# Kernel tuning notes

Measured on AMD Instinct MI355X. Metric: run time of the kernel, lower is better.

Reference implementation:

```python
import jax, jax.numpy as jnp
import numpy as np

HEAD_NUM = 8
KEY_DIM = 16
EMBEDDING_DIM = 128
LOGIT_CLIPPING = 10.0

B, G, P, E = 512, 100, 100, 128


def setup_inputs() -> dict:
    key = jax.random.key(0)
    ks = jax.random.split(key, 9)
    return {
        "input1": jax.random.normal(ks[0], (B, 1, E), jnp.float32),
        "input2": jax.random.normal(ks[1], (B, G, E), jnp.float32),
        "remaining_loaded": jax.random.uniform(ks[2], (B, G, 1), jnp.float32),
        "ninf_mask": jnp.zeros((B, G, P), jnp.float32),
        "encoded_nodes": jax.random.normal(ks[3], (B, P, E), jnp.float32),
        "Wq": jax.random.normal(ks[4], (2 * E + 1, HEAD_NUM * KEY_DIM), jnp.float32) * 0.05,
        "Wk": jax.random.normal(ks[5], (E, HEAD_NUM * KEY_DIM), jnp.float32) * 0.05,
        "Wv": jax.random.normal(ks[6], (E, HEAD_NUM * KEY_DIM), jnp.float32) * 0.05,
        "Wc": jax.random.normal(ks[7], (HEAD_NUM * KEY_DIM, E), jnp.float32) * 0.05,
        "bc": jnp.zeros((E,), jnp.float32),
    }


def _heads(x):  # [B, N, H*K] -> [B, H, N, K]
    b, n, _ = x.shape
    return x.reshape(b, n, HEAD_NUM, KEY_DIM).transpose(0, 2, 1, 3)


def reference(input1, input2, remaining_loaded, ninf_mask, encoded_nodes, Wq, Wk, Wv, Wc, bc):
    group_s = input2.shape[1]
    # reset(): precompute keys/values from encoded nodes
    k = _heads(encoded_nodes @ Wk)  # [B,H,P,K]
    v = _heads(encoded_nodes @ Wv)  # [B,H,P,K]
    # forward()
    input_cat = jnp.concatenate(
        [jnp.broadcast_to(input1, (input1.shape[0], group_s, input1.shape[2])),
         input2, remaining_loaded], axis=2)  # [B,G,2E+1]
    q = _heads(input_cat @ Wq)  # [B,H,G,K]
    # multi-head attention with additive ninf mask
    score = jnp.einsum("bhgk,bhpk->bhgp", q, k) / np.sqrt(KEY_DIM).astype(np.float32)
    score = score + ninf_mask[:, None, :, :]
    weights = jax.nn.softmax(score, axis=3)
    out = jnp.einsum("bhgp,bhpk->bhgk", weights, v)  # [B,H,G,K]
    out_concat = out.transpose(0, 2, 1, 3).reshape(out.shape[0], group_s, HEAD_NUM * KEY_DIM)
    mh_atten_out = out_concat @ Wc + bc  # [B,G,E]
    # single-head pointer scoring with tanh clipping
    score2 = jnp.einsum("bge,bpe->bgp", mh_atten_out, encoded_nodes) / np.sqrt(EMBEDDING_DIM).astype(np.float32)
    score_masked = LOGIT_CLIPPING * jnp.tanh(score2) + ninf_mask
    probs = jax.nn.softmax(score_masked, axis=2)
    return probs
```

## Files before the change

### kernel.cpp

```cpp
#include <hip/hip_runtime.h>

#define NB 512
#define NG 100
#define NP 100
#define NE 128
#define NH 8
#define LDST 136

typedef __attribute__((ext_vector_type(8))) short short8;
typedef __attribute__((ext_vector_type(4))) short short4v;
typedef __attribute__((ext_vector_type(4))) float f32x4;

__device__ __forceinline__ short f2bf(float f) {
    union { float f; unsigned u; } v; v.f = f;
    unsigned r = v.u + 0x7FFFu + ((v.u >> 16) & 1u);
    return (short)(r >> 16);
}

__global__ void prep_kernel(const float* __restrict__ Wq, const float* __restrict__ Wk,
                            const float* __restrict__ Wv, const float* __restrict__ Wc,
                            short* __restrict__ WqT2, short* __restrict__ WkT,
                            short* __restrict__ WvT, short* __restrict__ WcT,
                            float* __restrict__ wqlast)
{
    int idx = blockIdx.x * 256 + threadIdx.x;
    int mat = idx >> 14;
    int e   = idx & 16383;
    int k = e >> 7, n = e & 127;
    float v;
    short* dst;
    if (mat == 0)      { v = Wq[(128 + k) * 128 + n]; dst = WqT2; }
    else if (mat == 1) { v = Wk[k * 128 + n];         dst = WkT;  }
    else if (mat == 2) { v = Wv[k * 128 + n];         dst = WvT;  }
    else               { v = Wc[k * 128 + n];         dst = WcT;  }
    dst[n * 128 + k] = f2bf(v);
    if (idx < 128) wqlast[idx] = Wq[256 * 128 + idx];
}

__global__ __launch_bounds__(512, 2)
void fused_kernel(const float* __restrict__ input1, const float* __restrict__ input2,
                  const float* __restrict__ rem, const float* __restrict__ mask,
                  const float* __restrict__ enc, const float* __restrict__ Wq,
                  const float* __restrict__ bc,
                  const short* __restrict__ WqT2, const short* __restrict__ WkT,
                  const short* __restrict__ WvT, const short* __restrict__ WcT,
                  const float* __restrict__ wqlast, float* __restrict__ out)
{
    extern __shared__ short smem[];
    short* sEnc = smem;
    short* sK   = sEnc + 100 * LDST;
    short* sQ   = sK   + 100 * LDST;
    short* sVT  = sQ   + 100 * LDST;
    short* sWs  = sVT  + 128 * LDST;
    float* sQ1  = (float*)(sWs + 8 * 16 * LDST);

    const int b    = blockIdx.x;
    const int tid  = threadIdx.x;
    const int wave = tid >> 6, lane = tid & 63;
    const int l16  = lane & 15, lh = lane >> 4;

    {
        const float4* e4 = (const float4*)(enc    + (size_t)b * NP * NE);
        const float4* i4 = (const float4*)(input2 + (size_t)b * NG * NE);
        for (int idx = tid; idx < 100 * 32; idx += 512) {
            int row = idx >> 5, c = idx & 31;
            float4 v = e4[idx];
            short4v h = { f2bf(v.x), f2bf(v.y), f2bf(v.z), f2bf(v.w) };
            *(short4v*)(sEnc + row * LDST + c * 4) = h;
            float4 w = i4[idx];
            short4v h2 = { f2bf(w.x), f2bf(w.y), f2bf(w.z), f2bf(w.w) };
            *(short4v*)(sVT + row * LDST + c * 4) = h2;
        }
        {
            int n = tid & 127, part = tid >> 7;
            const float* i1 = input1 + (size_t)b * NE;
            float s = 0.f;
            #pragma unroll 8
            for (int k = part * 32; k < part * 32 + 32; ++k)
                s += i1[k] * Wq[k * NE + n];
            sQ1[part * 128 + n] = s;
        }
    }
    __syncthreads();

    for (int t = wave; t < 56; t += 8) {
        int mt = t >> 3, nt = t & 7;
        f32x4 acc = {0.f, 0.f, 0.f, 0.f};
        #pragma unroll
        for (int ks = 0; ks < 4; ++ks) {
            short8 a = *(const short8*)(sVT + (mt * 16 + l16) * LDST + ks * 32 + lh * 8);
            short8 w = *(const short8*)(WqT2 + (nt * 16 + l16) * NE + ks * 32 + lh * 8);
            acc = __builtin_amdgcn_mfma_f32_16x16x32_bf16(a, w, acc, 0, 0, 0);
        }
        int n = nt * 16 + l16;
        float q1n = sQ1[n] + sQ1[128 + n] + sQ1[256 + n] + sQ1[384 + n];
        float wl = wqlast[n];
        #pragma unroll
        for (int r = 0; r < 4; ++r) {
            int g = mt * 16 + lh * 4 + r;
            if (g < NG) {
                float rv = rem[(size_t)b * NG + g];
                sQ[g * LDST + n] = f2bf(acc[r] + q1n + rv * wl);
            }
        }
    }
    __syncthreads();

    for (int t = wave; t < 112; t += 8) {
        int isV = t >= 56;
        int tt = t - (isV ? 56 : 0);
        int mt = tt >> 3, nt = tt & 7;
        const short* WT = isV ? WvT : WkT;
        f32x4 acc = {0.f, 0.f, 0.f, 0.f};
        #pragma unroll
        for (int ks = 0; ks < 4; ++ks) {
            short8 a = *(const short8*)(sEnc + (mt * 16 + l16) * LDST + ks * 32 + lh * 8);
            short8 w = *(const short8*)(WT + (nt * 16 + l16) * NE + ks * 32 + lh * 8);
            acc = __builtin_amdgcn_mfma_f32_16x16x32_bf16(a, w, acc, 0, 0, 0);
        }
        int n = nt * 16 + l16;
        if (!isV) {
            #pragma unroll
            for (int r = 0; r < 4; ++r) {
                int p = mt * 16 + lh * 4 + r;
                if (p < NP) sK[p * LDST + n] = f2bf(acc[r]);
            }
        } else {
            int p0 = mt * 16 + lh * 4;
            if (p0 < NP) {
                short4v h = { f2bf(acc[0]), f2bf(acc[1]), f2bf(acc[2]), f2bf(acc[3]) };
                *(short4v*)(sVT + n * LDST + p0) = h;
            }
        }
    }
    for (int idx = tid; idx < 128 * 36; idx += 512) {
        int n = idx / 36, c = 100 + idx % 36;
        sVT[n * LDST + c] = 0;
    }
    __syncthreads();

    float mk[7][4];
    if (wave < 7) {
        const int gt = wave;
        #pragma unroll
        for (int pt = 0; pt < 7; ++pt)
            #pragma unroll
            for (int r = 0; r < 4; ++r) {
                int g = gt * 16 + lh * 4 + r, p = pt * 16 + l16;
                mk[pt][r] = (g < NG && p < NP) ? mask[((size_t)b * NG + g) * NP + p]
                                               : -__builtin_inff();
            }
        short* myW = sWs + wave * 16 * LDST;
        for (int i = lane; i < 16 * 24; i += 64) {
            int rr = i / 24, c = 112 + i % 24;
            myW[rr * LDST + c] = 0;
        }

        for (int h = 0; h < NH; ++h) {
            short8 aq = {0,0,0,0,0,0,0,0};
            if (lh < 2) aq = *(const short8*)(sQ + (gt * 16 + l16) * LDST + h * 16 + lh * 8);
            f32x4 sc[7];
            #pragma unroll
            for (int pt = 0; pt < 7; ++pt) {
                short8 kk = {0,0,0,0,0,0,0,0};
                if (lh < 2) kk = *(const short8*)(sK + (pt * 16 + l16) * LDST + h * 16 + lh * 8);
                f32x4 z = {0.f, 0.f, 0.f, 0.f};
                sc[pt] = __builtin_amdgcn_mfma_f32_16x16x32_bf16(aq, kk, z, 0, 0, 0);
            }
            float vals[7][4];
            #pragma unroll
            for (int pt = 0; pt < 7; ++pt) {
                bool pv = (pt * 16 + l16) < NP;
                #pragma unroll
                for (int r = 0; r < 4; ++r)
                    vals[pt][r] = pv ? sc[pt][r] * 0.25f + mk[pt][r] : -__builtin_inff();
            }
            #pragma unroll
            for (int r = 0; r < 4; ++r) {
                float m = vals[0][r];
                #pragma unroll
                for (int pt = 1; pt < 7; ++pt) m = fmaxf(m, vals[pt][r]);
                #pragma unroll
                for (int d = 1; d < 16; d <<= 1) m = fmaxf(m, __shfl_xor(m, d, 64));
                float s = 0.f;
                #pragma unroll
                for (int pt = 0; pt < 7; ++pt) {
                    float e = ((pt * 16 + l16) < NP) ? __expf(vals[pt][r] - m) : 0.f;
                    vals[pt][r] = e; s += e;
                }
                #pragma unroll
                for (int d = 1; d < 16; d <<= 1) s += __shfl_xor(s, d, 64);
                float inv = 1.f / s;
                #pragma unroll
                for (int pt = 0; pt < 7; ++pt) vals[pt][r] *= inv;
            }
            #pragma unroll
            for (int pt = 0; pt < 7; ++pt)
                #pragma unroll
                for (int r = 0; r < 4; ++r)
                    myW[(lh * 4 + r) * LDST + pt * 16 + l16] = f2bf(vals[pt][r]);
            f32x4 o = {0.f, 0.f, 0.f, 0.f};
            #pragma unroll
            for (int ps = 0; ps < 4; ++ps) {
                short8 a  = *(const short8*)(myW + l16 * LDST + ps * 32 + lh * 8);
                short8 vv = *(const short8*)(sVT + (h * 16 + l16) * LDST + ps * 32 + lh * 8);
                o = __builtin_amdgcn_mfma_f32_16x16x32_bf16(a, vv, o, 0, 0, 0);
            }
            #pragma unroll
            for (int r = 0; r < 4; ++r) {
                int g = gt * 16 + lh * 4 + r;
                if (g < NG) sQ[g * LDST + h * 16 + l16] = f2bf(o[r]);
            }
        }
    }
    __syncthreads();

    for (int t = wave; t < 56; t += 8) {
        int mt = t >> 3, nt = t & 7;
        f32x4 acc = {0.f, 0.f, 0.f, 0.f};
        #pragma unroll
        for (int ks = 0; ks < 4; ++ks) {
            short8 a = *(const short8*)(sQ + (mt * 16 + l16) * LDST + ks * 32 + lh * 8);
            short8 w = *(const short8*)(WcT + (nt * 16 + l16) * NE + ks * 32 + lh * 8);
            acc = __builtin_amdgcn_mfma_f32_16x16x32_bf16(a, w, acc, 0, 0, 0);
        }
        int n = nt * 16 + l16;
        float bias = bc[n];
        #pragma unroll
        for (int r = 0; r < 4; ++r) {
            int g = mt * 16 + lh * 4 + r;
            if (g < NG) sK[g * LDST + n] = f2bf(acc[r] + bias);
        }
    }
    __syncthreads();

    if (wave < 7) {
        const int gt = wave;
        short8 afr[4];
        #pragma unroll
        for (int ks = 0; ks < 4; ++ks)
            afr[ks] = *(const short8*)(sK + (gt * 16 + l16) * LDST + ks * 32 + lh * 8);
        float vals[7][4];
        #pragma unroll
        for (int pt = 0; pt < 7; ++pt) {
            f32x4 acc = {0.f, 0.f, 0.f, 0.f};
            #pragma unroll
            for (int ks = 0; ks < 4; ++ks) {
                short8 e8 = *(const short8*)(sEnc + (pt * 16 + l16) * LDST + ks * 32 + lh * 8);
                acc = __builtin_amdgcn_mfma_f32_16x16x32_bf16(afr[ks], e8, acc, 0, 0, 0);
            }
            bool pv = (pt * 16 + l16) < NP;
            #pragma unroll
            for (int r = 0; r < 4; ++r) {
                float x = acc[r] * 0.08838834764831845f;
                float th = 1.f - 2.f / (__expf(2.f * x) + 1.f);
                vals[pt][r] = pv ? 10.f * th + mk[pt][r] : -__builtin_inff();
            }
        }
        #pragma unroll
        for (int r = 0; r < 4; ++r) {
            float m = vals[0][r];
            #pragma unroll
            for (int pt = 1; pt < 7; ++pt) m = fmaxf(m, vals[pt][r]);
            #pragma unroll
            for (int d = 1; d < 16; d <<= 1) m = fmaxf(m, __shfl_xor(m, d, 64));
            float s = 0.f;
            #pragma unroll
            for (int pt = 0; pt < 7; ++pt) {
                float e = ((pt * 16 + l16) < NP) ? __expf(vals[pt][r] - m) : 0.f;
                vals[pt][r] = e; s += e;
            }
            #pragma unroll
            for (int d = 1; d < 16; d <<= 1) s += __shfl_xor(s, d, 64);
            float inv = 1.f / s;
            #pragma unroll
            for (int pt = 0; pt < 7; ++pt) vals[pt][r] *= inv;
        }
        #pragma unroll
        for (int pt = 0; pt < 7; ++pt) {
            int p = pt * 16 + l16;
            if (p < NP) {
                #pragma unroll
                for (int r = 0; r < 4; ++r) {
                    int g = gt * 16 + lh * 4 + r;
                    if (g < NG) out[((size_t)b * NG + g) * NP + p] = vals[pt][r];
                }
            }
        }
    }
}

#define SMEM_BYTES ((3 * 100 * LDST + 128 * LDST + 8 * 16 * LDST) * 2 + 512 * 4)

extern "C" void kernel_launch(void* const* d_in, const int* in_sizes, int n_in,
                              void* d_out, int out_size, void* d_ws, size_t ws_size,
                              hipStream_t stream)
{
    const float* input1 = (const float*)d_in[0];
    const float* input2 = (const float*)d_in[1];
    const float* rem    = (const float*)d_in[2];
    const float* mask   = (const float*)d_in[3];
    const float* enc    = (const float*)d_in[4];
    const float* Wq     = (const float*)d_in[5];
    const float* Wk     = (const float*)d_in[6];
    const float* Wv     = (const float*)d_in[7];
    const float* Wc     = (const float*)d_in[8];
    const float* bc     = (const float*)d_in[9];

    short* WqT2   = (short*)d_ws;
    short* WkT    = WqT2 + 16384;
    short* WvT    = WkT + 16384;
    short* WcT    = WvT + 16384;
    float* wqlast = (float*)(WcT + 16384);

    prep_kernel<<<256, 256, 0, stream>>>(Wq, Wk, Wv, Wc, WqT2, WkT, WvT, WcT, wqlast);

    hipFuncSetAttribute((const void*)fused_kernel,
                        hipFuncAttributeMaxDynamicSharedMemorySize, SMEM_BYTES);
    fused_kernel<<<NB, 512, SMEM_BYTES, stream>>>(
        input1, input2, rem, mask, enc, Wq, bc,
        WqT2, WkT, WvT, WcT, wqlast, (float*)d_out);
}
```

Before: 210.4 us.

## Keep per-wave Q/attention/output in registers with transposed MFMA and swizzled LDS

Result: slower. 321.5 us (+52.8%).

```diff
diff --git a/kernel.cpp b/kernel.cpp
--- a/kernel.cpp
+++ b/kernel.cpp
@@ -5,11 +5,19 @@
 #define NP 100
 #define NE 128
 #define NH 8
-#define LDST 136
 
 typedef __attribute__((ext_vector_type(8))) short short8;
 typedef __attribute__((ext_vector_type(4))) short short4v;
 typedef __attribute__((ext_vector_type(4))) float f32x4;
+
+#define SE_STRIDE 128
+#define SK_STRIDE 128
+#define SVT_STRIDE 112
+#define SE_BASE 0
+#define SK_BASE (100 * 128)
+#define SVT_BASE (SK_BASE + 100 * 128)
+#define SMEM_SHORTS (SVT_BASE + 128 * 112)
+#define SMEM_BYTES (SMEM_SHORTS * 2 + 256 * 4)
 
 __device__ __forceinline__ short f2bf(float f) {
     union { float f; unsigned u; } v; v.f = f;
@@ -17,11 +25,27 @@
     return (short)(r >> 16);
 }
 
+__device__ __forceinline__ f32x4 mfma16(short4v a, short4v b, f32x4 c) {
+#if __has_builtin(__builtin_amdgcn_mfma_f32_16x16x16_bf16)
+    return __builtin_amdgcn_mfma_f32_16x16x16_bf16(a, b, c, 0, 0, 0);
+#elif __has_builtin(__builtin_amdgcn_mfma_f32_16x16x16bf16_1k)
+    return __builtin_amdgcn_mfma_f32_16x16x16bf16_1k(a, b, c, 0, 0, 0);
+#else
+    f32x4 d;
+    asm volatile("v_mfma_f32_16x16x16_bf16 %0, %1, %2, %3"
+                 : "=&v"(d) : "v"(a), "v"(b), "v"(c));
+    return d;
+#endif
+}
+
+__device__ __forceinline__ f32x4 mfma32(short8 a, short8 b, f32x4 c) {
+    return __builtin_amdgcn_mfma_f32_16x16x32_bf16(a, b, c, 0, 0, 0);
+}
+
 __global__ void prep_kernel(const float* __restrict__ Wq, const float* __restrict__ Wk,
                             const float* __restrict__ Wv, const float* __restrict__ Wc,
                             short* __restrict__ WqT2, short* __restrict__ WkT,
-                            short* __restrict__ WvT, short* __restrict__ WcT,
-                            float* __restrict__ wqlast)
+                            short* __restrict__ WvT, short* __restrict__ WcT)
 {
     int idx = blockIdx.x * 256 + threadIdx.x;
     int mat = idx >> 14;
@@ -34,263 +58,253 @@
     else if (mat == 2) { v = Wv[k * 128 + n];         dst = WvT;  }
     else               { v = Wc[k * 128 + n];         dst = WcT;  }
     dst[n * 128 + k] = f2bf(v);
-    if (idx < 128) wqlast[idx] = Wq[256 * 128 + idx];
-}
-
-__global__ __launch_bounds__(512, 2)
+}
+
+__global__ __launch_bounds__(448, 4)
 void fused_kernel(const float* __restrict__ input1, const float* __restrict__ input2,
                   const float* __restrict__ rem, const float* __restrict__ mask,
                   const float* __restrict__ enc, const float* __restrict__ Wq,
                   const float* __restrict__ bc,
                   const short* __restrict__ WqT2, const short* __restrict__ WkT,
                   const short* __restrict__ WvT, const short* __restrict__ WcT,
-                  const float* __restrict__ wqlast, float* __restrict__ out)
+                  float* __restrict__ out)
 {
     extern __shared__ short smem[];
-    short* sEnc = smem;
-    short* sK   = sEnc + 100 * LDST;
-    short* sQ   = sK   + 100 * LDST;
-    short* sVT  = sQ   + 100 * LDST;
-    short* sWs  = sVT  + 128 * LDST;
-    float* sQ1  = (float*)(sWs + 8 * 16 * LDST);
+    float* sQ1 = (float*)(smem + SMEM_SHORTS);
 
     const int b    = blockIdx.x;
     const int tid  = threadIdx.x;
     const int wave = tid >> 6, lane = tid & 63;
     const int l16  = lane & 15, lh = lane >> 4;
+    const int gt   = wave;
+    const int g    = gt * 16 + l16;
+    const bool gok = (g < NG);
+    const float NINF = -__builtin_inff();
 
     {
-        const float4* e4 = (const float4*)(enc    + (size_t)b * NP * NE);
-        const float4* i4 = (const float4*)(input2 + (size_t)b * NG * NE);
-        for (int idx = tid; idx < 100 * 32; idx += 512) {
+        const f32x4* e4 = (const f32x4*)(enc + (size_t)b * NP * NE);
+        for (int idx = tid; idx < NP * 32; idx += 448) {
             int row = idx >> 5, c = idx & 31;
-            float4 v = e4[idx];
-            short4v h = { f2bf(v.x), f2bf(v.y), f2bf(v.z), f2bf(v.w) };
-            *(short4v*)(sEnc + row * LDST + c * 4) = h;
-            float4 w = i4[idx];
-            short4v h2 = { f2bf(w.x), f2bf(w.y), f2bf(w.z), f2bf(w.w) };
-            *(short4v*)(sVT + row * LDST + c * 4) = h2;
-        }
-        {
-            int n = tid & 127, part = tid >> 7;
-            const float* i1 = input1 + (size_t)b * NE;
+            f32x4 v = e4[idx];
+            short4v h = { f2bf(v[0]), f2bf(v[1]), f2bf(v[2]), f2bf(v[3]) };
+            int off = (row * SE_STRIDE + c * 4) ^ ((row & 15) << 2);
+            *(short4v*)(smem + SE_BASE + off) = h;
+        }
+        for (int idx = tid; idx < 128 * 3; idx += 448) {
+            int row = idx / 3, c = 100 + (idx % 3) * 4;
+            int off = (row * SVT_STRIDE + c) ^ ((row & 15) << 2);
+            *(short4v*)(smem + SVT_BASE + off) = (short4v){0, 0, 0, 0};
+        }
+        if (tid < 256) {
+            int part = tid >> 7, n = tid & 127;
+            const float* i1 = input1 + (size_t)b * NE + part * 64;
+            const float* wq = Wq + (size_t)part * 64 * NE + n;
             float s = 0.f;
             #pragma unroll 8
-            for (int k = part * 32; k < part * 32 + 32; ++k)
-                s += i1[k] * Wq[k * NE + n];
+            for (int k = 0; k < 64; ++k) s += i1[k] * wq[k * NE];
             sQ1[part * 128 + n] = s;
         }
     }
     __syncthreads();
 
-    for (int t = wave; t < 56; t += 8) {
-        int mt = t >> 3, nt = t & 7;
+    for (int t = wave; t < 112; t += 7) {
+        int mat = (t >= 56);
+        int tt  = mat ? t - 56 : t;
+        int mt = tt >> 3, nt = tt & 7;
+        const short* WT = mat ? WvT : WkT;
+        int arow = mt * 16 + l16;
+        bool aok = (arow < NP);
         f32x4 acc = {0.f, 0.f, 0.f, 0.f};
         #pragma unroll
-        for (int ks = 0; ks < 4; ++ks) {
-            short8 a = *(const short8*)(sVT + (mt * 16 + l16) * LDST + ks * 32 + lh * 8);
-            short8 w = *(const short8*)(WqT2 + (nt * 16 + l16) * NE + ks * 32 + lh * 8);
-            acc = __builtin_amdgcn_mfma_f32_16x16x32_bf16(a, w, acc, 0, 0, 0);
-        }
-        int n = nt * 16 + l16;
-        float q1n = sQ1[n] + sQ1[128 + n] + sQ1[256 + n] + sQ1[384 + n];
-        float wl = wqlast[n];
-        #pragma unroll
-        for (int r = 0; r < 4; ++r) {
-            int g = mt * 16 + lh * 4 + r;
-            if (g < NG) {
-                float rv = rem[(size_t)b * NG + g];
-                sQ[g * LDST + n] = f2bf(acc[r] + q1n + rv * wl);
-            }
-        }
-    }
-    __syncthreads();
-
-    for (int t = wave; t < 112; t += 8) {
-        int isV = t >= 56;
-        int tt = t - (isV ? 56 : 0);
-        int mt = tt >> 3, nt = tt & 7;
-        const short* WT = isV ? WvT : WkT;
-        f32x4 acc = {0.f, 0.f, 0.f, 0.f};
-        #pragma unroll
-        for (int ks = 0; ks < 4; ++ks) {
-            short8 a = *(const short8*)(sEnc + (mt * 16 + l16) * LDST + ks * 32 + lh * 8);
-            short8 w = *(const short8*)(WT + (nt * 16 + l16) * NE + ks * 32 + lh * 8);
-            acc = __builtin_amdgcn_mfma_f32_16x16x32_bf16(a, w, acc, 0, 0, 0);
-        }
-        int n = nt * 16 + l16;
-        if (!isV) {
+        for (int kt = 0; kt < 8; ++kt) {
+            short4v a = {0, 0, 0, 0};
+            if (aok) {
+                int off = (arow * SE_STRIDE + kt * 16 + lh * 4) ^ ((arow & 15) << 2);
+                a = *(const short4v*)(smem + SE_BASE + off);
+            }
+            short4v w = *(const short4v*)(WT + (nt * 16 + l16) * NE + kt * 16 + lh * 4);
+            acc = mfma16(a, w, acc);
+        }
+        if (!mat) {
             #pragma unroll
             for (int r = 0; r < 4; ++r) {
                 int p = mt * 16 + lh * 4 + r;
-                if (p < NP) sK[p * LDST + n] = f2bf(acc[r]);
+                if (p < NP) {
+                    int off = (p * SK_STRIDE + nt * 16 + l16) ^ ((p & 15) << 2);
+                    smem[SK_BASE + off] = f2bf(acc[r]);
+                }
             }
         } else {
+            int vrow = nt * 16 + l16;
             int p0 = mt * 16 + lh * 4;
             if (p0 < NP) {
                 short4v h = { f2bf(acc[0]), f2bf(acc[1]), f2bf(acc[2]), f2bf(acc[3]) };
-                *(short4v*)(sVT + n * LDST + p0) = h;
-            }
-        }
-    }
-    for (int idx = tid; idx < 128 * 36; idx += 512) {
-        int n = idx / 36, c = 100 + idx % 36;
-        sVT[n * LDST + c] = 0;
+                int off = (vrow * SVT_STRIDE + p0) ^ ((vrow & 15) << 2);
+                *(short4v*)(smem + SVT_BASE + off) = h;
+            }
+        }
+    }
+
+    short4v qb[8];
+    {
+        const float* xrow = input2 + ((size_t)b * NG + g) * NE;
+        short8 xb[4];
+        #pragma unroll
+        for (int ks = 0; ks < 4; ++ks) {
+            f32x4 v0 = {0.f,0.f,0.f,0.f}, v1 = {0.f,0.f,0.f,0.f};
+            if (gok) {
+                v0 = *(const f32x4*)(xrow + ks * 32 + lh * 8);
+                v1 = *(const f32x4*)(xrow + ks * 32 + lh * 8 + 4);
+            }
+            xb[ks] = (short8){ f2bf(v0[0]), f2bf(v0[1]), f2bf(v0[2]), f2bf(v0[3]),
+                               f2bf(v1[0]), f2bf(v1[1]), f2bf(v1[2]), f2bf(v1[3]) };
+        }
+        float remv = gok ? rem[(size_t)b * NG + g] : 0.f;
+        #pragma unroll
+        for (int nt = 0; nt < 8; ++nt) {
+            f32x4 acc = {0.f, 0.f, 0.f, 0.f};
+            #pragma unroll
+            for (int ks = 0; ks < 4; ++ks) {
+                short8 a = *(const short8*)(WqT2 + (nt * 16 + l16) * NE + ks * 32 + lh * 8);
+                acc = mfma32(a, xb[ks], acc);
+            }
+            f32x4 q1a = *(const f32x4*)(sQ1 + nt * 16 + lh * 4);
+            f32x4 q1b = *(const f32x4*)(sQ1 + 128 + nt * 16 + lh * 4);
+            f32x4 wlv = *(const f32x4*)(Wq + 256 * NE + nt * 16 + lh * 4);
+            short4v q;
+            #pragma unroll
+            for (int r = 0; r < 4; ++r)
+                q[r] = f2bf(0.25f * (acc[r] + q1a[r] + q1b[r] + remv * wlv[r]));
+            qb[nt] = q;
+        }
+    }
+
+    float mk[7][4];
+    {
+        const float* mrow = mask + ((size_t)b * NG + g) * NP;
+        #pragma unroll
+        for (int pt = 0; pt < 7; ++pt)
+            #pragma unroll
+            for (int r = 0; r < 4; ++r) {
+                int p = pt * 16 + lh * 4 + r;
+                mk[pt][r] = (gok && p < NP) ? mrow[p] : NINF;
+            }
     }
     __syncthreads();
 
-    float mk[7][4];
-    if (wave < 7) {
-        const int gt = wave;
-        #pragma unroll
-        for (int pt = 0; pt < 7; ++pt)
-            #pragma unroll
-            for (int r = 0; r < 4; ++r) {
-                int g = gt * 16 + lh * 4 + r, p = pt * 16 + l16;
-                mk[pt][r] = (g < NG && p < NP) ? mask[((size_t)b * NG + g) * NP + p]
-                                               : -__builtin_inff();
-            }
-        short* myW = sWs + wave * 16 * LDST;
-        for (int i = lane; i < 16 * 24; i += 64) {
-            int rr = i / 24, c = 112 + i % 24;
-            myW[rr * LDST + c] = 0;
-        }
-
-        for (int h = 0; h < NH; ++h) {
-            short8 aq = {0,0,0,0,0,0,0,0};
-            if (lh < 2) aq = *(const short8*)(sQ + (gt * 16 + l16) * LDST + h * 16 + lh * 8);
-            f32x4 sc[7];
-            #pragma unroll
-            for (int pt = 0; pt < 7; ++pt) {
-                short8 kk = {0,0,0,0,0,0,0,0};
-                if (lh < 2) kk = *(const short8*)(sK + (pt * 16 + l16) * LDST + h * 16 + lh * 8);
-                f32x4 z = {0.f, 0.f, 0.f, 0.f};
-                sc[pt] = __builtin_amdgcn_mfma_f32_16x16x32_bf16(aq, kk, z, 0, 0, 0);
-            }
-            float vals[7][4];
-            #pragma unroll
-            for (int pt = 0; pt < 7; ++pt) {
-                bool pv = (pt * 16 + l16) < NP;
-                #pragma unroll
-                for (int r = 0; r < 4; ++r)
-                    vals[pt][r] = pv ? sc[pt][r] * 0.25f + mk[pt][r] : -__builtin_inff();
-            }
-            #pragma unroll
-            for (int r = 0; r < 4; ++r) {
-                float m = vals[0][r];
-                #pragma unroll
-                for (int pt = 1; pt < 7; ++pt) m = fmaxf(m, vals[pt][r]);
-                #pragma unroll
-                for (int d = 1; d < 16; d <<= 1) m = fmaxf(m, __shfl_xor(m, d, 64));
-                float s = 0.f;
-                #pragma unroll
-                for (int pt = 0; pt < 7; ++pt) {
-                    float e = ((pt * 16 + l16) < NP) ? __expf(vals[pt][r] - m) : 0.f;
-                    vals[pt][r] = e; s += e;
-                }
-                #pragma unroll
-                for (int d = 1; d < 16; d <<= 1) s += __shfl_xor(s, d, 64);
-                float inv = 1.f / s;
-                #pragma unroll
-                for (int pt = 0; pt < 7; ++pt) vals[pt][r] *= inv;
-            }
-            #pragma unroll
-            for (int pt = 0; pt < 7; ++pt)
-                #pragma unroll
-                for (int r = 0; r < 4; ++r)
-                    myW[(lh * 4 + r) * LDST + pt * 16 + l16] = f2bf(vals[pt][r]);
-            f32x4 o = {0.f, 0.f, 0.f, 0.f};
-            #pragma unroll
-            for (int ps = 0; ps < 4; ++ps) {
-                short8 a  = *(const short8*)(myW + l16 * LDST + ps * 32 + lh * 8);
-                short8 vv = *(const short8*)(sVT + (h * 16 + l16) * LDST + ps * 32 + lh * 8);
-                o = __builtin_amdgcn_mfma_f32_16x16x32_bf16(a, vv, o, 0, 0, 0);
-            }
-            #pragma unroll
-            for (int r = 0; r < 4; ++r) {
-                int g = gt * 16 + lh * 4 + r;
-                if (g < NG) sQ[g * LDST + h * 16 + l16] = f2bf(o[r]);
-            }
-        }
-    }
-    __syncthreads();
-
-    for (int t = wave; t < 56; t += 8) {
-        int mt = t >> 3, nt = t & 7;
+    short4v ocb[8];
+    #pragma unroll
+    for (int h = 0; h < NH; ++h) {
+        f32x4 sc[7];
+        #pragma unroll
+        for (int pt = 0; pt < 7; ++pt) {
+            int prow = pt * 16 + l16;
+            int off = (prow * SK_STRIDE + h * 16 + lh * 4) ^ ((prow & 15) << 2);
+            short4v kf = *(const short4v*)(smem + SK_BASE + off);
+            f32x4 z = {0.f, 0.f, 0.f, 0.f};
+            sc[pt] = mfma16(kf, qb[h], z);
+        }
+        float vals[7][4];
+        float m = NINF;
+        #pragma unroll
+        for (int pt = 0; pt < 7; ++pt)
+            #pragma unroll
+            for (int r = 0; r < 4; ++r) {
+                bool pv = (pt < 6) || (lh == 0);
+                float v = pv ? sc[pt][r] + mk[pt][r] : NINF;
+                vals[pt][r] = v;
+                m = fmaxf(m, v);
+            }
+        m = fmaxf(m, __shfl_xor(m, 16));
+        m = fmaxf(m, __shfl_xor(m, 32));
+        float s = 0.f;
+        #pragma unroll
+        for (int pt = 0; pt < 7; ++pt)
+            #pragma unroll
+            for (int r = 0; r < 4; ++r) {
+                float e = __expf(vals[pt][r] - m);
+                vals[pt][r] = e; s += e;
+            }
+        s += __shfl_xor(s, 16);
+        s += __shfl_xor(s, 32);
+        float inv = 1.f / s;
+        f32x4 o = {0.f, 0.f, 0.f, 0.f};
+        #pragma unroll
+        for (int pt = 0; pt < 7; ++pt) {
+            short4v pb = { f2bf(vals[pt][0] * inv), f2bf(vals[pt][1] * inv),
+                           f2bf(vals[pt][2] * inv), f2bf(vals[pt][3] * inv) };
+            int vrow = h * 16 + l16;
+            int off = (vrow * SVT_STRIDE + pt * 16 + lh * 4) ^ ((vrow & 15) << 2);
+            short4v vf = *(const short4v*)(smem + SVT_BASE + off);
+            o = mfma16(vf, pb, o);
+        }
+        ocb[h] = (short4v){ f2bf(o[0]), f2bf(o[1]), f2bf(o[2]), f2bf(o[3]) };
+    }
+
+    short4v mhb[8];
+    #pragma unroll
+    for (int nt = 0; nt < 8; ++nt) {
         f32x4 acc = {0.f, 0.f, 0.f, 0.f};
         #pragma unroll
-        for (int ks = 0; ks < 4; ++ks) {
-            short8 a = *(const short8*)(sQ + (mt * 16 + l16) * LDST + ks * 32 + lh * 8);
-            short8 w = *(const short8*)(WcT + (nt * 16 + l16) * NE + ks * 32 + lh * 8);
-            acc = __builtin_amdgcn_mfma_f32_16x16x32_bf16(a, w, acc, 0, 0, 0);
-        }
-        int n = nt * 16 + l16;
-        float bias = bc[n];
+        for (int kt = 0; kt < 8; ++kt) {
+            short4v a = *(const short4v*)(WcT + (nt * 16 + l16) * NE + kt * 16 + lh * 4);
+            acc = mfma16(a, ocb[kt], acc);
+        }
+        f32x4 bcv = *(const f32x4*)(bc + nt * 16 + lh * 4);
+        mhb[nt] = (short4v){ f2bf((acc[0] + bcv[0]) * 0.08838834764831845f),
+                             f2bf((acc[1] + bcv[1]) * 0.08838834764831845f),
+                             f2bf((acc[2] + bcv[2]) * 0.08838834764831845f),
+                             f2bf((acc[3] + bcv[3]) * 0.08838834764831845f) };
+    }
+
+    float vals2[7][4];
+    #pragma unroll
+    for (int pt = 0; pt < 7; ++pt) {
+        int prow = pt * 16 + l16;
+        f32x4 acc = {0.f, 0.f, 0.f, 0.f};
+        #pragma unroll
+        for (int kt = 0; kt < 8; ++kt) {
+            int off = (prow * SE_STRIDE + kt * 16 + lh * 4) ^ ((prow & 15) << 2);
+            short4v ef = *(const short4v*)(smem + SE_BASE + off);
+            acc = mfma16(ef, mhb[kt], acc);
+        }
         #pragma unroll
         for (int r = 0; r < 4; ++r) {
-            int g = mt * 16 + lh * 4 + r;
-            if (g < NG) sK[g * LDST + n] = f2bf(acc[r] + bias);
-        }
-    }
-    __syncthreads();
-
-    if (wave < 7) {
-        const int gt = wave;
-        short8 afr[4];
-        #pragma unroll
-        for (int ks = 0; ks < 4; ++ks)
-            afr[ks] = *(const short8*)(sK + (gt * 16 + l16) * LDST + ks * 32 + lh * 8);
-        float vals[7][4];
-        #pragma unroll
-        for (int pt = 0; pt < 7; ++pt) {
-            f32x4 acc = {0.f, 0.f, 0.f, 0.f};
-            #pragma unroll
-            for (int ks = 0; ks < 4; ++ks) {
-                short8 e8 = *(const short8*)(sEnc + (pt * 16 + l16) * LDST + ks * 32 + lh * 8);
-                acc = __builtin_amdgcn_mfma_f32_16x16x32_bf16(afr[ks], e8, acc, 0, 0, 0);
-            }
-            bool pv = (pt * 16 + l16) < NP;
-            #pragma unroll
-            for (int r = 0; r < 4; ++r) {
-                float x = acc[r] * 0.08838834764831845f;
-                float th = 1.f - 2.f / (__expf(2.f * x) + 1.f);
-                vals[pt][r] = pv ? 10.f * th + mk[pt][r] : -__builtin_inff();
-            }
-        }
-        #pragma unroll
-        for (int r = 0; r < 4; ++r) {
-            float m = vals[0][r];
-            #pragma unroll
-            for (int pt = 1; pt < 7; ++pt) m = fmaxf(m, vals[pt][r]);
-            #pragma unroll
-            for (int d = 1; d < 16; d <<= 1) m = fmaxf(m, __shfl_xor(m, d, 64));
-            float s = 0.f;
-            #pragma unroll
-            for (int pt = 0; pt < 7; ++pt) {
-                float e = ((pt * 16 + l16) < NP) ? __expf(vals[pt][r] - m) : 0.f;
-                vals[pt][r] = e; s += e;
-            }
-            #pragma unroll
-            for (int d = 1; d < 16; d <<= 1) s += __shfl_xor(s, d, 64);
-            float inv = 1.f / s;
-            #pragma unroll
-            for (int pt = 0; pt < 7; ++pt) vals[pt][r] *= inv;
-        }
-        #pragma unroll
-        for (int pt = 0; pt < 7; ++pt) {
-            int p = pt * 16 + l16;
-            if (p < NP) {
-                #pragma unroll
-                for (int r = 0; r < 4; ++r) {
-                    int g = gt * 16 + lh * 4 + r;
-                    if (g < NG) out[((size_t)b * NG + g) * NP + p] = vals[pt][r];
-                }
-            }
-        }
-    }
-}
-
-#define SMEM_BYTES ((3 * 100 * LDST + 128 * LDST + 8 * 16 * LDST) * 2 + 512 * 4)
+            bool pv = (pt < 6) || (lh == 0);
+            float x = acc[r];
+            float th = 1.f - 2.f / (__expf(2.f * x) + 1.f);
+            vals2[pt][r] = pv ? 10.f * th + mk[pt][r] : NINF;
+        }
+    }
+    {
+        float m = NINF;
+        #pragma unroll
+        for (int pt = 0; pt < 7; ++pt)
+            #pragma unroll
+            for (int r = 0; r < 4; ++r) m = fmaxf(m, vals2[pt][r]);
+        m = fmaxf(m, __shfl_xor(m, 16));
+        m = fmaxf(m, __shfl_xor(m, 32));
+        float s = 0.f;
+        #pragma unroll
+        for (int pt = 0; pt < 7; ++pt)
+            #pragma unroll
+            for (int r = 0; r < 4; ++r) {
+                float e = __expf(vals2[pt][r] - m);
+                vals2[pt][r] = e; s += e;
+            }
+        s += __shfl_xor(s, 16);
+        s += __shfl_xor(s, 32);
+        float inv = 1.f / s;
+        float* orow = out + ((size_t)b * NG + g) * NP;
+        #pragma unroll
+        for (int pt = 0; pt < 7; ++pt)
+            #pragma unroll
+            for (int r = 0; r < 4; ++r) {
+                int p = pt * 16 + lh * 4 + r;
+                if (gok && p < NP) orow[p] = vals2[pt][r] * inv;
+            }
+    }
+}
 
 extern "C" void kernel_launch(void* const* d_in, const int* in_sizes, int n_in,
                               void* d_out, int out_size, void* d_ws, size_t ws_size,
@@ -307,17 +321,16 @@
     const float* Wc     = (const float*)d_in[8];
     const float* bc     = (const float*)d_in[9];
 
-    short* WqT2   = (short*)d_ws;
-    short* WkT    = WqT2 + 16384;
-    short* WvT    = WkT + 16384;
-    short* WcT    = WvT + 16384;
-    float* wqlast = (float*)(WcT + 16384);
-
-    prep_kernel<<<256, 256, 0, stream>>>(Wq, Wk, Wv, Wc, WqT2, WkT, WvT, WcT, wqlast);
+    short* WqT2 = (short*)d_ws;
+    short* WkT  = WqT2 + 16384;
+    short* WvT  = WkT + 16384;
+    short* WcT  = WvT + 16384;
+
+    prep_kernel<<<256, 256, 0, stream>>>(Wq, Wk, Wv, Wc, WqT2, WkT, WvT, WcT);
 
     hipFuncSetAttribute((const void*)fused_kernel,
                         hipFuncAttributeMaxDynamicSharedMemorySize, SMEM_BYTES);
-    fused_kernel<<<NB, 512, SMEM_BYTES, stream>>>(
+    fused_kernel<<<NB, 448, SMEM_BYTES, stream>>>(
         input1, input2, rem, mask, enc, Wq, bc,
-        WqT2, WkT, WvT, WcT, wqlast, (float*)d_out);
-}
+        WqT2, WkT, WvT, WcT, (float*)d_out);
+}
```
